# Performance work log

Hardware: AMD Instinct MI355X
Metric: run time of the kernel (lower is better)

Reference implementation:

```python
import jax, jax.numpy as jnp
import numpy as np

NUM_CLASSES = 10
MARGIN = 1.0


def setup_inputs() -> dict:
    key = jax.random.key(0)
    k1, k2 = jax.random.split(key)
    N, D = 8192, 128
    embeddings = jax.random.normal(k1, (N, D), dtype=jnp.float32)
    labels = jax.random.randint(k2, (N,), 0, NUM_CLASSES)
    return {"embeddings": embeddings, "labels": labels}


def _batch_hard_loss(embeddings, labels):
    # embeddings: [N, D] float, labels: [N] int in [0, NUM_CLASSES)
    N = embeddings.shape[0]
    x2 = jnp.sum(embeddings * embeddings, axis=1)  # [N]
    # squared euclidean pairwise distances via gram trick, clamped at 0
    d = jnp.maximum(x2[:, None] + x2[None, :] - 2.0 * (embeddings @ embeddings.T), 0.0)  # [N, N]
    same = labels[:, None] == labels[None, :]  # [N, N]

    # hardest positive: max squared distance over same-class (includes self, as in source)
    d_pos = jnp.max(jnp.where(same, d, -jnp.inf), axis=1)  # [N]

    # FAITHFUL TO SOURCE BUG: negative_distances[k] = sum_{j: label_j != k} d(i, j)
    # = T_i - S_i(k), where S_i(k) = sum over class-k members of d(i, j)
    onehot = jax.nn.one_hot(labels, NUM_CLASSES, dtype=d.dtype)  # [N, 10]
    S = d @ onehot  # [N, 10]
    T = jnp.sum(d, axis=1)  # [N]
    neg_dist = T[:, None] - S  # [N, 10]
    k_star = jnp.argmin(neg_dist, axis=1)  # [N], values in [0, 10)

    # negatives list for class c is ordered by (class, then index); take the k_star-th element
    order = jnp.argsort(labels * N + jnp.arange(N))  # global (class, index) order
    mask_sorted = (~same)[:, order]  # [N, N] negatives of anchor i, in list order
    cs = jnp.cumsum(mask_sorted.astype(jnp.int32), axis=1)
    cond = mask_sorted & (cs == (k_star[:, None] + 1))
    pos_in_sorted = jnp.argmax(cond, axis=1)  # first position with rank k_star
    j_star = order[pos_in_sorted]  # [N] index of the "worst negative"
    d_neg = d[jnp.arange(N), j_star]  # [N]

    # base TripletLoss: relu(d_pos - d_neg + margin); mean over batch (use_gt_than_zero_mean=False)
    loss = jax.nn.relu(d_pos - d_neg + MARGIN)
    return jnp.mean(loss)


def reference(embeddings, labels):
    return _batch_hard_loss(embeddings, labels)
```

## Files before the change

### kernel.cpp

```cpp
#include <hip/hip_runtime.h>
#include <hip/hip_bf16.h>

#define BH_N 8192
#define BH_D 128
#define BH_NC 10
#define BH_MARGIN 1.0f
#define NSEG 4
#define MAXTILES (BH_N / 32 + BH_NC)

typedef __attribute__((ext_vector_type(8)))  short bf16x8;
typedef __attribute__((ext_vector_type(16))) float f32x16;

#define OFF_R(r) (((r) & 3) + 8 * ((r) >> 2))

__device__ __forceinline__ unsigned short f2bf(float f) {
    unsigned u = __float_as_uint(f);
    u += 0x7fffu + ((u >> 16) & 1u);
    return (unsigned short)(u >> 16);
}
__device__ __forceinline__ float bf2f(short h) {
    return __uint_as_float(((unsigned)(unsigned short)h) << 16);
}

__global__ __launch_bounds__(1024) void bh_sort(const int* __restrict__ labels,
                                                int* __restrict__ perm,
                                                int* __restrict__ labs,
                                                int* __restrict__ cstart,
                                                int* __restrict__ zreg,
                                                float* __restrict__ out) {
    const int t = threadIdx.x;
    for (int i = t; i < BH_NC * BH_D + 16 + BH_N; i += 1024) zreg[i] = 0;
    if (t == 0) out[0] = 0.0f;

    const int lane = t & 63, w = t >> 6;
    const int4* lp = (const int4*)labels;
    const int4 a = lp[t * 2], b = lp[t * 2 + 1];
    int L[8] = {a.x, a.y, a.z, a.w, b.x, b.y, b.z, b.w};

    int lh[BH_NC];
#pragma unroll
    for (int c = 0; c < BH_NC; c++) lh[c] = 0;
#pragma unroll
    for (int k = 0; k < 8; k++) {
#pragma unroll
        for (int c = 0; c < BH_NC; c++) lh[c] += (L[k] == c);
    }
    int inc[BH_NC];
#pragma unroll
    for (int c = 0; c < BH_NC; c++) inc[c] = lh[c];
#pragma unroll
    for (int m = 1; m < 64; m <<= 1) {
#pragma unroll
        for (int c = 0; c < BH_NC; c++) {
            const int o = __shfl_up(inc[c], m);
            if (lane >= m) inc[c] += o;
        }
    }
    __shared__ int wtot[16][BH_NC];
    __shared__ int wpref[16][BH_NC];
    __shared__ int ctot[BH_NC];
    __shared__ int cst[BH_NC + 1];
    if (lane == 63) {
#pragma unroll
        for (int c = 0; c < BH_NC; c++) wtot[w][c] = inc[c];
    }
    __syncthreads();
    if (t < BH_NC) {
        int run = 0;
#pragma unroll
        for (int w2 = 0; w2 < 16; w2++) { wpref[w2][t] = run; run += wtot[w2][t]; }
        ctot[t] = run;
    }
    __syncthreads();
    if (t == 0) {
        int run = 0;
#pragma unroll
        for (int c = 0; c < BH_NC; c++) { cst[c] = run; run += ctot[c]; }
        cst[BH_NC] = run;
#pragma unroll
        for (int c = 0; c <= BH_NC; c++) cstart[c] = cst[c];
    }
    __syncthreads();
    int wpre[BH_NC];
#pragma unroll
    for (int c = 0; c < BH_NC; c++) wpre[c] = cst[c] + wpref[w][c] + inc[c] - lh[c];
#pragma unroll
    for (int k = 0; k < 8; k++) {
        const int j = t * 8 + k;
        const int Lk = L[k];
        int pos = 0;
#pragma unroll
        for (int c = 0; c < BH_NC; c++) pos += (Lk == c) ? wpre[c] : 0;
        perm[pos] = j;
        labs[pos] = Lk;
#pragma unroll
        for (int c = 0; c < BH_NC; c++) wpre[c] += (Lk == c);
    }
}

__global__ __launch_bounds__(512) void bh_permute(const float* __restrict__ E,
                                                  const int* __restrict__ perm,
                                                  const int* __restrict__ labs,
                                                  unsigned short* __restrict__ Es,
                                                  float* __restrict__ x2s,
                                                  float* __restrict__ M,
                                                  float* __restrict__ sumx2) {
    __shared__ float vbuf[16][132];
    __shared__ float x2r[16];
    __shared__ int lab16[16];
    const int t = threadIdx.x;
    const int r = t >> 5, sub = t & 31;
    const int row = blockIdx.x * 16 + r;
    const int oi = perm[row];
    const float4 v = ((const float4*)(E + (size_t)oi * BH_D))[sub];
    ushort4 h;
    h.x = f2bf(v.x); h.y = f2bf(v.y); h.z = f2bf(v.z); h.w = f2bf(v.w);
    ((ushort4*)(Es + (size_t)row * BH_D))[sub] = h;
    *(float4*)(&vbuf[r][sub * 4]) = v;
    float s = v.x * v.x + v.y * v.y + v.z * v.z + v.w * v.w;
#pragma unroll
    for (int m = 1; m < 32; m <<= 1) s += __shfl_xor(s, m);
    if (sub == 0) { x2s[row] = s; x2r[r] = s; lab16[r] = labs[row]; }
    __syncthreads();
    if (t < BH_D) {
        int c = lab16[0]; float acc = 0.0f;
#pragma unroll
        for (int rr = 0; rr < 16; rr++) {
            const int cr = lab16[rr];
            if (cr != c) { atomicAdd(&M[(size_t)c * BH_D + t], acc); acc = 0.0f; c = cr; }
            acc += vbuf[rr][t];
        }
        atomicAdd(&M[(size_t)c * BH_D + t], acc);
    } else if (t == BH_D) {
        int c = lab16[0]; float a2 = 0.0f;
#pragma unroll
        for (int rr = 0; rr < 16; rr++) {
            const int cr = lab16[rr];
            if (cr != c) { atomicAdd(&sumx2[c], a2); a2 = 0.0f; c = cr; }
            a2 += x2r[rr];
        }
        atomicAdd(&sumx2[c], a2);
    }
}

__global__ __launch_bounds__(64) void bh_dpos(const unsigned short* __restrict__ Es,
                                              const float* __restrict__ x2s,
                                              const int* __restrict__ cstart,
                                              int* __restrict__ dposU) {
    const int tile = blockIdx.x / NSEG;
    const int seg  = blockIdx.x % NSEG;
    int cs[BH_NC + 1];
#pragma unroll
    for (int c = 0; c <= BH_NC; c++) cs[c] = cstart[c];
    int c = -1, t0 = 0, base = 0;
#pragma unroll
    for (int cc = 0; cc < BH_NC; cc++) {
        const int len = cs[cc + 1] - cs[cc];
        const int nt = (len + 31) >> 5;
        if (c < 0 && tile < base + nt) { c = cc; t0 = tile - base; }
        base += nt;
    }
    if (c < 0) return;
    const int c0 = cs[c], c1 = cs[c + 1], len = c1 - c0;
    const int rb = c0 + t0 * 32;
    const int nch = (len + 31) >> 5;
    const int per = (nch + NSEG - 1) / NSEG;
    const int jb0 = c0 + seg * per * 32;
    if (jb0 >= c1) return;
    const int jb1 = min(jb0 + per * 32, c1);

    const int lane = threadIdx.x;
    const int cid = lane & 31, half = lane >> 5;
    const int rowbase = rb + 4 * half;

    bf16x8 afrag[8];
    {
        const int ar = min(rb + cid, BH_N - 1);
        const unsigned short* arow = Es + (size_t)ar * BH_D + half * 8;
#pragma unroll
        for (int ks = 0; ks < 8; ks++) afrag[ks] = *(const bf16x8*)(arow + ks * 16);
    }
    float xr[16];
#pragma unroll
    for (int r = 0; r < 16; r++) xr[r] = x2s[min(rowbase + OFF_R(r), BH_N - 1)];

    float dpos[16];
#pragma unroll
    for (int r = 0; r < 16; r++) dpos[r] = 0.0f;

    int jcl = min(jb0 + cid, c1 - 1);
    bf16x8 bcur[8];
    {
        const unsigned short* brow = Es + (size_t)jcl * BH_D + half * 8;
#pragma unroll
        for (int ks = 0; ks < 8; ks++) bcur[ks] = *(const bf16x8*)(brow + ks * 16);
    }
    float xc = x2s[jcl];

    for (int jb = jb0; jb < jb1; jb += 32) {
        const int jcln = min(jb + 32 + cid, c1 - 1);
        bf16x8 bnxt[8];
        {
            const unsigned short* brow = Es + (size_t)jcln * BH_D + half * 8;
#pragma unroll
            for (int ks = 0; ks < 8; ks++) bnxt[ks] = *(const bf16x8*)(brow + ks * 16);
        }
        const float xcn = x2s[jcln];

        f32x16 acc = {0.0f, 0.0f, 0.0f, 0.0f, 0.0f, 0.0f, 0.0f, 0.0f,
                      0.0f, 0.0f, 0.0f, 0.0f, 0.0f, 0.0f, 0.0f, 0.0f};
#pragma unroll
        for (int ks = 0; ks < 8; ks++)
            acc = __builtin_amdgcn_mfma_f32_32x32x16_bf16(afrag[ks], bcur[ks], acc, 0, 0, 0);

        const bool vm = (jb + cid) < jb1;
#pragma unroll
        for (int r = 0; r < 16; r++) {
            const float dd = fmaxf(fmaf(-2.0f, acc[r], xr[r] + xc), 0.0f);
            const bool rowin = (rowbase + OFF_R(r)) < c1;
            dpos[r] = fmaxf(dpos[r], (vm && rowin) ? dd : 0.0f);
        }
#pragma unroll
        for (int ks = 0; ks < 8; ks++) bcur[ks] = bnxt[ks];
        xc = xcn;
    }
#pragma unroll
    for (int r = 0; r < 16; r++) {
#pragma unroll
        for (int m = 1; m < 32; m <<= 1) dpos[r] = fmaxf(dpos[r], __shfl_xor(dpos[r], m));
    }
    if (cid == 0) {
#pragma unroll
        for (int r = 0; r < 16; r++) {
            const int row = rowbase + OFF_R(r);
            if (row < c1) atomicMax(&dposU[row], __float_as_int(dpos[r]));
        }
    }
}

__global__ __launch_bounds__(64) void bh_select(const unsigned short* __restrict__ Es,
                                                const float* __restrict__ x2s,
                                                const int* __restrict__ cstart,
                                                const float* __restrict__ M,
                                                const float* __restrict__ sumx2,
                                                const int* __restrict__ dposU,
                                                float* __restrict__ out) {
    const int lane = threadIdx.x;
    const int spos = blockIdx.x * 64 + lane;

    int cs[BH_NC + 1];
#pragma unroll
    for (int c = 0; c <= BH_NC; c++) cs[c] = cstart[c];

    bf16x8 u0[16];
    const unsigned short* rp = Es + (size_t)spos * BH_D;
#pragma unroll
    for (int k = 0; k < 16; k++) u0[k] = *(const bf16x8*)(rp + k * 8);

    float dc[BH_NC];
#pragma unroll
    for (int c = 0; c < BH_NC; c++) dc[c] = 0.0f;
#pragma unroll
    for (int k = 0; k < 16; k++) {
        float ef[8];
#pragma unroll
        for (int d = 0; d < 8; d++) ef[d] = bf2f(u0[k][d]);
#pragma unroll
        for (int c = 0; c < BH_NC; c++) {
            const float4 m0 = *(const float4*)(M + (size_t)c * BH_D + k * 8);
            const float4 m1 = *(const float4*)(M + (size_t)c * BH_D + k * 8 + 4);
            dc[c] += ef[0] * m0.x + ef[1] * m0.y + ef[2] * m0.z + ef[3] * m0.w
                   + ef[4] * m1.x + ef[5] * m1.y + ef[6] * m1.z + ef[7] * m1.w;
        }
    }

    const float x2i = x2s[spos];
    float T = 0.0f, Sk[BH_NC];
#pragma unroll
    for (int c = 0; c < BH_NC; c++) {
        Sk[c] = (float)(cs[c + 1] - cs[c]) * x2i + sumx2[c] - 2.0f * dc[c];
        T += Sk[c];
    }
    int kstar = 0; float best = T - Sk[0];
#pragma unroll
    for (int c = 1; c < BH_NC; c++) {
        const float nd = T - Sk[c];
        if (nd < best) { best = nd; kstar = c; }
    }

    int a = 0;
#pragma unroll
    for (int c = 1; c < BH_NC; c++) a += (spos >= cs[c]);
    const int p = (kstar < cs[a]) ? kstar : (cs[a + 1] + (kstar - cs[a]));

    const unsigned short* qp = Es + (size_t)p * BH_D;
    float dp = 0.0f;
#pragma unroll
    for (int k = 0; k < 16; k++) {
        const bf16x8 u1 = *(const bf16x8*)(qp + k * 8);
#pragma unroll
        for (int d = 0; d < 8; d++) dp += bf2f(u0[k][d]) * bf2f(u1[d == 0 ? 0 : d]);
    }
    dp = 0.0f;
#pragma unroll
    for (int k = 0; k < 16; k++) {
        const bf16x8 u1 = *(const bf16x8*)(qp + k * 8);
#pragma unroll
        for (int d = 0; d < 8; d++) dp = fmaf(bf2f(u0[k][d]), bf2f(u1[d]), dp);
    }
    const float dneg = fmaxf(x2i + x2s[p] - 2.0f * dp, 0.0f);

    const float dposv = __int_as_float(dposU[spos]);
    float loss = fmaxf(dposv - dneg + BH_MARGIN, 0.0f);
#pragma unroll
    for (int m = 1; m < 64; m <<= 1) loss += __shfl_xor(loss, m);
    if (lane == 0) atomicAdd(out, loss * (1.0f / (float)BH_N));
}

extern "C" void kernel_launch(void* const* d_in, const int* in_sizes, int n_in,
                              void* d_out, int out_size, void* d_ws, size_t ws_size,
                              hipStream_t stream) {
    const float* E = (const float*)d_in[0];
    const int* labels = (const int*)d_in[1];
    float* out = (float*)d_out;

    unsigned short* Es = (unsigned short*)d_ws;
    float* x2s   = (float*)(Es + (size_t)BH_N * BH_D);
    float* M     = x2s + BH_N;
    float* sumx2 = M + BH_NC * BH_D;
    int*   dposU = (int*)(sumx2 + 16);
    int*   perm  = dposU + BH_N;
    int*   labs  = perm + BH_N;
    int*   cstart= labs + BH_N;

    bh_sort<<<1, 1024, 0, stream>>>(labels, perm, labs, cstart, (int*)M, out);
    bh_permute<<<BH_N / 16, 512, 0, stream>>>(E, perm, labs, Es, x2s, M, sumx2);
    bh_dpos<<<MAXTILES * NSEG, 64, 0, stream>>>(Es, x2s, cstart, dposU);
    bh_select<<<BH_N / 64, 64, 0, stream>>>(Es, x2s, cstart, M, sumx2, dposU, out);
}
```

Before: 106.1 us.

## Convert embeddings unpermuted in parallel and gather via sort index

The old path ran a single-block sort, then a permute kernel that gathered rows into class order and accumulated per-class sums with global atomics. The new path converts embeddings to bf16 in their original order across many blocks. In parallel, it computes per-chunk class sums and squared norms without global atomics. A single-block kernel then reduces those partials, builds a sorted index in shared memory, and the distance kernels read rows indirectly through that index. This shortens the serial chain in front of the parallel work and removes atomic contention, but it adds an index indirection and scattered row reads in the MFMA and select kernels.

After: 114.6 us. 1.08x slower.

```diff
diff --git a/kernel.cpp b/kernel.cpp
--- a/kernel.cpp
+++ b/kernel.cpp
@@ -7,6 +7,8 @@
 #define BH_MARGIN 1.0f
 #define NSEG 4
 #define MAXTILES (BH_N / 32 + BH_NC)
+#define NCHUNK 8
+#define CHROWS (BH_N / NCHUNK)
 
 typedef __attribute__((ext_vector_type(8)))  short bf16x8;
 typedef __attribute__((ext_vector_type(16))) float f32x16;
@@ -22,14 +24,102 @@
     return __uint_as_float(((unsigned)(unsigned short)h) << 16);
 }
 
-__global__ __launch_bounds__(1024) void bh_sort(const int* __restrict__ labels,
-                                                int* __restrict__ perm,
-                                                int* __restrict__ labs,
-                                                int* __restrict__ cstart,
-                                                int* __restrict__ zreg,
-                                                float* __restrict__ out) {
+__global__ __launch_bounds__(1024) void bh_prep(const float* __restrict__ E,
+                                                const int* __restrict__ labels,
+                                                unsigned short* __restrict__ Es,
+                                                float* __restrict__ x2s,
+                                                float* __restrict__ Mpart,
+                                                float* __restrict__ sxpart,
+                                                int* __restrict__ dposU) {
     const int t = threadIdx.x;
-    for (int i = t; i < BH_NC * BH_D + 16 + BH_N; i += 1024) zreg[i] = 0;
+    const int b = blockIdx.x;
+    if (b < 32) {
+        const int lr = t >> 2, sub = t & 3;
+        const int row = b * 256 + lr;
+        const float4* ep = (const float4*)(E + (size_t)row * BH_D + sub * 32);
+        float4 v[8];
+#pragma unroll
+        for (int k = 0; k < 8; k++) v[k] = ep[k];
+        float s = 0.0f;
+#pragma unroll
+        for (int k = 0; k < 8; k++)
+            s += v[k].x * v[k].x + v[k].y * v[k].y + v[k].z * v[k].z + v[k].w * v[k].w;
+        s += __shfl_xor(s, 1); s += __shfl_xor(s, 2);
+        if (sub == 0) x2s[row] = s;
+        ushort4* op = (ushort4*)(Es + (size_t)row * BH_D + sub * 32);
+#pragma unroll
+        for (int k = 0; k < 8; k++) {
+            ushort4 h;
+            h.x = f2bf(v[k].x); h.y = f2bf(v[k].y); h.z = f2bf(v[k].z); h.w = f2bf(v[k].w);
+            op[k] = h;
+        }
+        if (t < 256) dposU[b * 256 + t] = 0;
+    } else {
+        const int idx = b - 32;
+        const int c = idx >> 3, chunk = idx & 7;
+        const int lr = t >> 2, sub = t & 3;
+        const int lane = t & 63;
+        float acc[32];
+#pragma unroll
+        for (int d = 0; d < 32; d++) acc[d] = 0.0f;
+        float sx = 0.0f;
+#pragma unroll
+        for (int rr = 0; rr < 4; rr++) {
+            const int row = chunk * CHROWS + rr * 256 + lr;
+            if (labels[row] == c) {
+                const float4* ep = (const float4*)(E + (size_t)row * BH_D + sub * 32);
+#pragma unroll
+                for (int k = 0; k < 8; k++) {
+                    const float4 v = ep[k];
+                    acc[k * 4 + 0] += v.x; acc[k * 4 + 1] += v.y;
+                    acc[k * 4 + 2] += v.z; acc[k * 4 + 3] += v.w;
+                    sx += v.x * v.x + v.y * v.y + v.z * v.z + v.w * v.w;
+                }
+            }
+        }
+        __shared__ float Msh[BH_D];
+        __shared__ float sxsh;
+        if (t < BH_D) Msh[t] = 0.0f;
+        if (t == 0) sxsh = 0.0f;
+        __syncthreads();
+#pragma unroll
+        for (int d = 0; d < 32; d++) {
+            float a = acc[d];
+            a += __shfl_xor(a, 4); a += __shfl_xor(a, 8);
+            a += __shfl_xor(a, 16); a += __shfl_xor(a, 32);
+            if ((lane & 60) == 0) atomicAdd(&Msh[sub * 32 + d], a);
+        }
+        sx += __shfl_xor(sx, 1); sx += __shfl_xor(sx, 2);
+        sx += __shfl_xor(sx, 4); sx += __shfl_xor(sx, 8);
+        sx += __shfl_xor(sx, 16); sx += __shfl_xor(sx, 32);
+        if (lane == 0) atomicAdd(&sxsh, sx);
+        __syncthreads();
+        if (t < BH_D) Mpart[((size_t)chunk * BH_NC + c) * BH_D + t] = Msh[t];
+        if (t == 0) sxpart[chunk * BH_NC + c] = sxsh;
+    }
+}
+
+__global__ __launch_bounds__(1024) void bh_sortk(const int* __restrict__ labels,
+                                                 int* __restrict__ sidx,
+                                                 int* __restrict__ cstart,
+                                                 const float* __restrict__ Mpart,
+                                                 const float* __restrict__ sxpart,
+                                                 float* __restrict__ M,
+                                                 float* __restrict__ sumx2,
+                                                 float* __restrict__ out) {
+    const int t = threadIdx.x;
+    for (int i = t; i < BH_NC * BH_D; i += 1024) {
+        float s = 0.0f;
+#pragma unroll
+        for (int ch = 0; ch < NCHUNK; ch++) s += Mpart[(size_t)ch * BH_NC * BH_D + i];
+        M[i] = s;
+    }
+    if (t < BH_NC) {
+        float s = 0.0f;
+#pragma unroll
+        for (int ch = 0; ch < NCHUNK; ch++) s += sxpart[ch * BH_NC + t];
+        sumx2[t] = s;
+    }
     if (t == 0) out[0] = 0.0f;
 
     const int lane = t & 63, w = t >> 6;
@@ -60,6 +150,7 @@
     __shared__ int wpref[16][BH_NC];
     __shared__ int ctot[BH_NC];
     __shared__ int cst[BH_NC + 1];
+    __shared__ int sid[BH_N];
     if (lane == 63) {
 #pragma unroll
         for (int c = 0; c < BH_NC; c++) wtot[w][c] = inc[c];
@@ -91,60 +182,17 @@
         int pos = 0;
 #pragma unroll
         for (int c = 0; c < BH_NC; c++) pos += (Lk == c) ? wpre[c] : 0;
-        perm[pos] = j;
-        labs[pos] = Lk;
+        sid[pos] = j;
 #pragma unroll
         for (int c = 0; c < BH_NC; c++) wpre[c] += (Lk == c);
     }
-}
-
-__global__ __launch_bounds__(512) void bh_permute(const float* __restrict__ E,
-                                                  const int* __restrict__ perm,
-                                                  const int* __restrict__ labs,
-                                                  unsigned short* __restrict__ Es,
-                                                  float* __restrict__ x2s,
-                                                  float* __restrict__ M,
-                                                  float* __restrict__ sumx2) {
-    __shared__ float vbuf[16][132];
-    __shared__ float x2r[16];
-    __shared__ int lab16[16];
-    const int t = threadIdx.x;
-    const int r = t >> 5, sub = t & 31;
-    const int row = blockIdx.x * 16 + r;
-    const int oi = perm[row];
-    const float4 v = ((const float4*)(E + (size_t)oi * BH_D))[sub];
-    ushort4 h;
-    h.x = f2bf(v.x); h.y = f2bf(v.y); h.z = f2bf(v.z); h.w = f2bf(v.w);
-    ((ushort4*)(Es + (size_t)row * BH_D))[sub] = h;
-    *(float4*)(&vbuf[r][sub * 4]) = v;
-    float s = v.x * v.x + v.y * v.y + v.z * v.z + v.w * v.w;
-#pragma unroll
-    for (int m = 1; m < 32; m <<= 1) s += __shfl_xor(s, m);
-    if (sub == 0) { x2s[row] = s; x2r[r] = s; lab16[r] = labs[row]; }
     __syncthreads();
-    if (t < BH_D) {
-        int c = lab16[0]; float acc = 0.0f;
-#pragma unroll
-        for (int rr = 0; rr < 16; rr++) {
-            const int cr = lab16[rr];
-            if (cr != c) { atomicAdd(&M[(size_t)c * BH_D + t], acc); acc = 0.0f; c = cr; }
-            acc += vbuf[rr][t];
-        }
-        atomicAdd(&M[(size_t)c * BH_D + t], acc);
-    } else if (t == BH_D) {
-        int c = lab16[0]; float a2 = 0.0f;
-#pragma unroll
-        for (int rr = 0; rr < 16; rr++) {
-            const int cr = lab16[rr];
-            if (cr != c) { atomicAdd(&sumx2[c], a2); a2 = 0.0f; c = cr; }
-            a2 += x2r[rr];
-        }
-        atomicAdd(&sumx2[c], a2);
-    }
+    for (int i = t; i < BH_N; i += 1024) sidx[i] = sid[i];
 }
 
 __global__ __launch_bounds__(64) void bh_dpos(const unsigned short* __restrict__ Es,
                                               const float* __restrict__ x2s,
+                                              const int* __restrict__ sidx,
                                               const int* __restrict__ cstart,
                                               int* __restrict__ dposU) {
     const int tile = blockIdx.x / NSEG;
@@ -175,37 +223,37 @@
 
     bf16x8 afrag[8];
     {
-        const int ar = min(rb + cid, BH_N - 1);
+        const int ar = sidx[min(rb + cid, BH_N - 1)];
         const unsigned short* arow = Es + (size_t)ar * BH_D + half * 8;
 #pragma unroll
         for (int ks = 0; ks < 8; ks++) afrag[ks] = *(const bf16x8*)(arow + ks * 16);
     }
     float xr[16];
 #pragma unroll
-    for (int r = 0; r < 16; r++) xr[r] = x2s[min(rowbase + OFF_R(r), BH_N - 1)];
+    for (int r = 0; r < 16; r++) xr[r] = x2s[sidx[min(rowbase + OFF_R(r), BH_N - 1)]];
 
     float dpos[16];
 #pragma unroll
     for (int r = 0; r < 16; r++) dpos[r] = 0.0f;
 
-    int jcl = min(jb0 + cid, c1 - 1);
+    int jor = sidx[min(jb0 + cid, c1 - 1)];
     bf16x8 bcur[8];
     {
-        const unsigned short* brow = Es + (size_t)jcl * BH_D + half * 8;
+        const unsigned short* brow = Es + (size_t)jor * BH_D + half * 8;
 #pragma unroll
         for (int ks = 0; ks < 8; ks++) bcur[ks] = *(const bf16x8*)(brow + ks * 16);
     }
-    float xc = x2s[jcl];
+    float xc = x2s[jor];
 
     for (int jb = jb0; jb < jb1; jb += 32) {
-        const int jcln = min(jb + 32 + cid, c1 - 1);
+        const int jorn = sidx[min(jb + 32 + cid, c1 - 1)];
         bf16x8 bnxt[8];
         {
-            const unsigned short* brow = Es + (size_t)jcln * BH_D + half * 8;
+            const unsigned short* brow = Es + (size_t)jorn * BH_D + half * 8;
 #pragma unroll
             for (int ks = 0; ks < 8; ks++) bnxt[ks] = *(const bf16x8*)(brow + ks * 16);
         }
-        const float xcn = x2s[jcln];
+        const float xcn = x2s[jorn];
 
         f32x16 acc = {0.0f, 0.0f, 0.0f, 0.0f, 0.0f, 0.0f, 0.0f, 0.0f,
                       0.0f, 0.0f, 0.0f, 0.0f, 0.0f, 0.0f, 0.0f, 0.0f};
@@ -240,6 +288,7 @@
 
 __global__ __launch_bounds__(64) void bh_select(const unsigned short* __restrict__ Es,
                                                 const float* __restrict__ x2s,
+                                                const int* __restrict__ sidx,
                                                 const int* __restrict__ cstart,
                                                 const float* __restrict__ M,
                                                 const float* __restrict__ sumx2,
@@ -252,8 +301,9 @@
 #pragma unroll
     for (int c = 0; c <= BH_NC; c++) cs[c] = cstart[c];
 
+    const int oi = sidx[spos];
     bf16x8 u0[16];
-    const unsigned short* rp = Es + (size_t)spos * BH_D;
+    const unsigned short* rp = Es + (size_t)oi * BH_D;
 #pragma unroll
     for (int k = 0; k < 16; k++) u0[k] = *(const bf16x8*)(rp + k * 8);
 
@@ -274,7 +324,7 @@
         }
     }
 
-    const float x2i = x2s[spos];
+    const float x2i = x2s[oi];
     float T = 0.0f, Sk[BH_NC];
 #pragma unroll
     for (int c = 0; c < BH_NC; c++) {
@@ -292,23 +342,17 @@
 #pragma unroll
     for (int c = 1; c < BH_NC; c++) a += (spos >= cs[c]);
     const int p = (kstar < cs[a]) ? kstar : (cs[a + 1] + (kstar - cs[a]));
-
-    const unsigned short* qp = Es + (size_t)p * BH_D;
+    const int oj = sidx[p];
+
+    const unsigned short* qp = Es + (size_t)oj * BH_D;
     float dp = 0.0f;
 #pragma unroll
     for (int k = 0; k < 16; k++) {
         const bf16x8 u1 = *(const bf16x8*)(qp + k * 8);
 #pragma unroll
-        for (int d = 0; d < 8; d++) dp += bf2f(u0[k][d]) * bf2f(u1[d == 0 ? 0 : d]);
-    }
-    dp = 0.0f;
-#pragma unroll
-    for (int k = 0; k < 16; k++) {
-        const bf16x8 u1 = *(const bf16x8*)(qp + k * 8);
-#pragma unroll
         for (int d = 0; d < 8; d++) dp = fmaf(bf2f(u0[k][d]), bf2f(u1[d]), dp);
     }
-    const float dneg = fmaxf(x2i + x2s[p] - 2.0f * dp, 0.0f);
+    const float dneg = fmaxf(x2i + x2s[oj] - 2.0f * dp, 0.0f);
 
     const float dposv = __int_as_float(dposU[spos]);
     float loss = fmaxf(dposv - dneg + BH_MARGIN, 0.0f);
@@ -328,13 +372,14 @@
     float* x2s   = (float*)(Es + (size_t)BH_N * BH_D);
     float* M     = x2s + BH_N;
     float* sumx2 = M + BH_NC * BH_D;
-    int*   dposU = (int*)(sumx2 + 16);
-    int*   perm  = dposU + BH_N;
-    int*   labs  = perm + BH_N;
-    int*   cstart= labs + BH_N;
-
-    bh_sort<<<1, 1024, 0, stream>>>(labels, perm, labs, cstart, (int*)M, out);
-    bh_permute<<<BH_N / 16, 512, 0, stream>>>(E, perm, labs, Es, x2s, M, sumx2);
-    bh_dpos<<<MAXTILES * NSEG, 64, 0, stream>>>(Es, x2s, cstart, dposU);
-    bh_select<<<BH_N / 64, 64, 0, stream>>>(Es, x2s, cstart, M, sumx2, dposU, out);
-}
+    float* Mpart = sumx2 + 16;
+    float* sxpart= Mpart + (size_t)NCHUNK * BH_NC * BH_D;
+    int*   dposU = (int*)(sxpart + 128);
+    int*   sidx  = dposU + BH_N;
+    int*   cstart= sidx + BH_N;
+
+    bh_prep<<<112, 1024, 0, stream>>>(E, labels, Es, x2s, Mpart, sxpart, dposU);
+    bh_sortk<<<1, 1024, 0, stream>>>(labels, sidx, cstart, Mpart, sxpart, M, sumx2, out);
+    bh_dpos<<<MAXTILES * NSEG, 64, 0, stream>>>(Es, x2s, sidx, cstart, dposU);
+    bh_select<<<BH_N / 64, 64, 0, stream>>>(Es, x2s, sidx, cstart, M, sumx2, dposU, out);
+}
```
